# Kernel optimization log

Hardware: AMD Instinct MI355X
Metric: run time of the kernel (lower is better)

## Reference

```python
import jax, jax.numpy as jnp
import numpy as np

EPS = 1e-7  # keras backend epsilon
S = 64.0
M = 0.5
B, D, NC = 1024, 512, 50000


def setup_inputs() -> dict:
    key = jax.random.key(0)
    kx, kw, kl = jax.random.split(key, 3)
    x = jax.random.normal(kx, (B, D), dtype=jnp.float32)
    W = jax.random.normal(kw, (D, NC), dtype=jnp.float32)
    labels = jax.random.randint(kl, (B,), 0, NC)
    y = jax.nn.one_hot(labels, NC, dtype=jnp.float32)  # [B, NC] one-hot targets
    return {"x": x, "y": y, "W": W}


def reference(x, y, W):
    # L2-normalize embeddings (rows) and class weights (columns)
    xn = x / jnp.linalg.norm(x, axis=1, keepdims=True)
    Wn = W / jnp.linalg.norm(W, axis=0, keepdims=True)
    logits = xn @ Wn  # [B, NC] cosine similarities
    theta = jnp.arccos(jnp.clip(logits, -1.0 + EPS, 1.0 - EPS))
    target_logits = jnp.cos(theta + M)
    logits = logits * (1.0 - y) + target_logits * y
    logits = logits * S
    return jax.nn.softmax(logits, axis=-1)
```

## Files before the change

kernel.cpp:

```cpp
#include <hip/hip_runtime.h>
#include <hip/hip_fp16.h>
#include <cstdint>
#include <cstddef>

#define NCLS 50000
#define DIM 512
#define NROW 1024
#define NTN 391

typedef _Float16 half8 __attribute__((ext_vector_type(8)));
typedef float f32x4 __attribute__((ext_vector_type(4)));

#define AS1(p) ((const __attribute__((address_space(1))) void*)(p))
#define AS3(p) ((__attribute__((address_space(3))) void*)(p))

__global__ void prep_x_kernel(const float* __restrict__ x,
                              __half* __restrict__ xh,
                              float* __restrict__ rn)
{
    int row = blockIdx.x;
    int l = threadIdx.x;
    const float4* xr = (const float4*)(x + (size_t)row * DIM);
    __half2* dst = (__half2*)(xh + (size_t)row * DIM);
    float s = 0.f;
#pragma unroll
    for (int i = 0; i < 2; ++i) {
        int idx = l + i * 64;
        float4 v = xr[idx];
        dst[idx * 2]     = __floats2half2_rn(v.x, v.y);
        dst[idx * 2 + 1] = __floats2half2_rn(v.z, v.w);
        s += v.x * v.x + v.y * v.y + v.z * v.z + v.w * v.w;
    }
#pragma unroll
    for (int off = 32; off > 0; off >>= 1) s += __shfl_down(s, off);
    if (l == 0) rn[row] = rsqrtf(s);
}

__global__ void transpose_w_kernel(const float* __restrict__ W,
                                   __half* __restrict__ Wt,
                                   float* __restrict__ part)
{
    __shared__ float tile[64][65];
    __shared__ float cpart[4][64];
    int n0 = blockIdx.x * 64;
    int k0 = blockIdx.y * 64;
    int t = threadIdx.x;
    int f4 = t & 15;
    int kr = t >> 4;
    int n = n0 + f4 * 4;
    bool ok = (n < NCLS);
#pragma unroll
    for (int i = 0; i < 4; ++i) {
        int k = kr + i * 16;
        float4 v = ok ? *(const float4*)(W + (size_t)(k0 + k) * NCLS + n)
                      : make_float4(0.f, 0.f, 0.f, 0.f);
        tile[k][f4 * 4 + 0] = v.x;
        tile[k][f4 * 4 + 1] = v.y;
        tile[k][f4 * 4 + 2] = v.z;
        tile[k][f4 * 4 + 3] = v.w;
    }
    __syncthreads();
#pragma unroll
    for (int i = 0; i < 8; ++i) {
        int idx = t + i * 256;
        int nn = idx >> 5;
        int kp = idx & 31;
        int gn = n0 + nn;
        if (gn < NCLS) {
            __half2 h = __floats2half2_rn(tile[kp * 2][nn], tile[kp * 2 + 1][nn]);
            *(__half2*)(Wt + (size_t)gn * DIM + k0 + kp * 2) = h;
        }
    }
    {
        int nn = t & 63;
        int seg = t >> 6;
        float s = 0.f;
#pragma unroll
        for (int k = 0; k < 16; ++k) {
            float v = tile[seg * 16 + k][nn];
            s += v * v;
        }
        cpart[seg][nn] = s;
        __syncthreads();
        if (t < 64 && n0 + t < NCLS) {
            part[(size_t)blockIdx.y * NCLS + n0 + t] =
                cpart[0][t] + cpart[1][t] + cpart[2][t] + cpart[3][t];
        }
    }
}

__global__ void make_cn_kernel(const float* __restrict__ part, float* __restrict__ cn)
{
    int c = blockIdx.x * 256 + threadIdx.x;
    if (c >= NCLS) return;
    float s = 0.f;
#pragma unroll
    for (int j = 0; j < 8; ++j) s += part[(size_t)j * NCLS + c];
    cn[c] = rsqrtf(s);
}

__global__ void find_labels_kernel(const float4* __restrict__ y4, int* __restrict__ lab)
{
    int i4 = blockIdx.x * 256 + threadIdx.x;
    float4 v = y4[i4];
    if (v.x != 0.f || v.y != 0.f || v.z != 0.f || v.w != 0.f) {
        long base = (long)i4 * 4;
        if (v.x != 0.f) { long i = base + 0; lab[i / NCLS] = (int)(i % NCLS); }
        if (v.y != 0.f) { long i = base + 1; lab[i / NCLS] = (int)(i % NCLS); }
        if (v.z != 0.f) { long i = base + 2; lab[i / NCLS] = (int)(i % NCLS); }
        if (v.w != 0.f) { long i = base + 3; lab[i / NCLS] = (int)(i % NCLS); }
    }
}

template<int PASS>
__global__ __launch_bounds__(256, 4) void gemm_arc_kernel(
    const __half* __restrict__ A,
    const __half* __restrict__ Bt,
    const float* __restrict__ rn,
    const float* __restrict__ cn,
    const int* __restrict__ lab,
    const float* __restrict__ rs,
    float* __restrict__ out,
    float* __restrict__ rowpart)
{
    __shared__ __align__(16) __half As[128 * 64];
    __shared__ __align__(16) __half Bs[128 * 64];
    __shared__ float rsum[2][128];

    const int tid = threadIdx.x;
    const int wid = tid >> 6;
    const int lane = tid & 63;
    const int wm = wid >> 1;
    const int wn = wid & 1;

    const int b = blockIdx.x;
    const int w = (b & 7) * NTN + (b >> 3);
    const int mt = w & 7;
    const int nt = w >> 3;
    const int tileM = mt * 128;
    const int tileN = nt * 128;

    const int srow = lane >> 3;
    const int sblk = (lane & 7) ^ srow;

    f32x4 acc[4][4] = {};

    auto stage = [&](int k0) {
#pragma unroll
        for (int c = 0; c < 4; ++c) {
            int chunk = wid * 4 + c;
            int row = chunk * 8 + srow;
            const __half* sa = A + (size_t)(tileM + row) * DIM + k0 + sblk * 8;
            __builtin_amdgcn_global_load_lds(AS1(sa), AS3((char*)As + chunk * 1024), 16, 0, 0);
            int gn = tileN + row;
            if (gn > NCLS - 1) gn = NCLS - 1;
            const __half* sb = Bt + (size_t)gn * DIM + k0 + sblk * 8;
            __builtin_amdgcn_global_load_lds(AS1(sb), AS3((char*)Bs + chunk * 1024), 16, 0, 0);
        }
    };

    auto compute = [&]() {
        const int krow = lane >> 4;
        const int rl = lane & 15;
#pragma unroll
        for (int kk = 0; kk < 2; ++kk) {
            half8 af[4], bf[4];
#pragma unroll
            for (int m = 0; m < 4; ++m) {
                int r = wm * 64 + m * 16 + rl;
                int kb = (kk * 4 + krow) ^ (r & 7);
                af[m] = *(const half8*)((const char*)As + r * 128 + kb * 16);
            }
#pragma unroll
            for (int n = 0; n < 4; ++n) {
                int r = wn * 64 + n * 16 + rl;
                int kb = (kk * 4 + krow) ^ (r & 7);
                bf[n] = *(const half8*)((const char*)Bs + r * 128 + kb * 16);
            }
#pragma unroll
            for (int m = 0; m < 4; ++m)
#pragma unroll
                for (int n = 0; n < 4; ++n)
                    acc[m][n] = __builtin_amdgcn_mfma_f32_16x16x32_f16(af[m], bf[n], acc[m][n], 0, 0, 0);
        }
    };

#pragma unroll 1
    for (int k0 = 0; k0 < DIM; k0 += 64) {
        stage(k0);
        __syncthreads();
        compute();
        __syncthreads();
    }

    const float cosM = 0.8775825618903728f;
    const float sinM = 0.4794255386042030f;
    const int col_l = lane & 15;
    const int rgrp = lane >> 4;

#pragma unroll
    for (int m = 0; m < 4; ++m) {
        int gr0 = tileM + wm * 64 + m * 16 + rgrp * 4;
        float rnv[4]; int labv[4]; float rsv[4];
#pragma unroll
        for (int r = 0; r < 4; ++r) {
            rnv[r] = rn[gr0 + r];
            labv[r] = lab[gr0 + r];
            if (PASS == 1) rsv[r] = rs[gr0 + r];
        }
        float rowacc[4] = {0.f, 0.f, 0.f, 0.f};
#pragma unroll
        for (int n = 0; n < 4; ++n) {
            int gc = tileN + wn * 64 + n * 16 + col_l;
            bool okc = (gc < NCLS);
            float cnv = okc ? cn[gc] : 0.f;
#pragma unroll
            for (int r = 0; r < 4; ++r) {
                float cv = acc[m][n][r] * rnv[r] * cnv;
                float logit;
                if (gc == labv[r]) {
                    float cc = fminf(fmaxf(cv, -1.f + 1e-7f), 1.f - 1e-7f);
                    logit = 64.f * (cc * cosM - sqrtf(1.f - cc * cc) * sinM);
                } else {
                    logit = 64.f * cv;
                }
                float e = __expf(logit);
                if (PASS == 0) {
                    if (okc) rowacc[r] += e;
                } else {
                    if (okc) out[(size_t)(gr0 + r) * NCLS + gc] = e * rsv[r];
                }
            }
        }
        if (PASS == 0) {
#pragma unroll
            for (int r = 0; r < 4; ++r) {
                float s = rowacc[r];
                s += __shfl_xor(s, 1);
                s += __shfl_xor(s, 2);
                s += __shfl_xor(s, 4);
                s += __shfl_xor(s, 8);
                if (col_l == 0) rsum[wn][wm * 64 + m * 16 + rgrp * 4 + r] = s;
            }
        }
    }
    if (PASS == 0) {
        __syncthreads();
        if (tid < 128) {
            float tot = rsum[0][tid] + rsum[1][tid];
            rowpart[(size_t)nt * NROW + tileM + tid] = tot;
        }
    }
}

__global__ void reduce_rs_kernel(const float* __restrict__ rowpart, float* __restrict__ rs)
{
    int row = blockIdx.x * 256 + threadIdx.x;
    float s = 0.f;
    for (int t = 0; t < NTN; ++t) s += rowpart[(size_t)t * NROW + row];
    rs[row] = 1.f / s;
}

extern "C" void kernel_launch(void* const* d_in, const int* in_sizes, int n_in,
                              void* d_out, int out_size, void* d_ws, size_t ws_size,
                              hipStream_t stream)
{
    const float* x = (const float*)d_in[0];
    const float* y = (const float*)d_in[1];
    const float* W = (const float*)d_in[2];
    float* out = (float*)d_out;

    char* ws = (char*)d_ws;
    __half* Wt     = (__half*)(ws);
    __half* xh     = (__half*)(ws + 51200000);
    float* rn      = (float*) (ws + 52248576);
    float* cn      = (float*) (ws + 52252672);
    float* part    = (float*) (ws + 52452672);
    float* rowpart = part;
    int*   lab     = (int*)   (ws + 54054208);
    float* rs      = (float*) (ws + 54058304);

    hipLaunchKernelGGL(prep_x_kernel, dim3(NROW), dim3(64), 0, stream, x, xh, rn);
    hipLaunchKernelGGL(transpose_w_kernel, dim3(782, 8), dim3(256), 0, stream, W, Wt, part);
    hipLaunchKernelGGL(make_cn_kernel, dim3(196), dim3(256), 0, stream, part, cn);
    hipLaunchKernelGGL(find_labels_kernel, dim3(50000), dim3(256), 0, stream, (const float4*)y, lab);
    hipLaunchKernelGGL(gemm_arc_kernel<0>, dim3(8 * NTN), dim3(256), 0, stream,
                       xh, Wt, rn, cn, lab, rs, out, rowpart);
    hipLaunchKernelGGL(reduce_rs_kernel, dim3(4), dim3(256), 0, stream, rowpart, rs);
    hipLaunchKernelGGL(gemm_arc_kernel<1>, dim3(8 * NTN), dim3(256), 0, stream,
                       xh, Wt, rn, cn, lab, rs, out, rowpart);
}
```

Before: 257.7 us.

## Replace second GEMM pass with single pass plus separate normalization kernel

```diff
diff --git a/kernel.cpp b/kernel.cpp
--- a/kernel.cpp
+++ b/kernel.cpp
@@ -112,14 +112,12 @@
     }
 }
 
-template<int PASS>
 __global__ __launch_bounds__(256, 4) void gemm_arc_kernel(
     const __half* __restrict__ A,
     const __half* __restrict__ Bt,
     const float* __restrict__ rn,
     const float* __restrict__ cn,
     const int* __restrict__ lab,
-    const float* __restrict__ rs,
     float* __restrict__ out,
     float* __restrict__ rowpart)
 {
@@ -201,12 +199,11 @@
 #pragma unroll
     for (int m = 0; m < 4; ++m) {
         int gr0 = tileM + wm * 64 + m * 16 + rgrp * 4;
-        float rnv[4]; int labv[4]; float rsv[4];
+        float rnv[4]; int labv[4];
 #pragma unroll
         for (int r = 0; r < 4; ++r) {
             rnv[r] = rn[gr0 + r];
             labv[r] = lab[gr0 + r];
-            if (PASS == 1) rsv[r] = rs[gr0 + r];
         }
         float rowacc[4] = {0.f, 0.f, 0.f, 0.f};
 #pragma unroll
@@ -225,31 +222,26 @@
                     logit = 64.f * cv;
                 }
                 float e = __expf(logit);
-                if (PASS == 0) {
-                    if (okc) rowacc[r] += e;
-                } else {
-                    if (okc) out[(size_t)(gr0 + r) * NCLS + gc] = e * rsv[r];
+                if (okc) {
+                    rowacc[r] += e;
+                    out[(size_t)(gr0 + r) * NCLS + gc] = e;
                 }
             }
         }
-        if (PASS == 0) {
-#pragma unroll
-            for (int r = 0; r < 4; ++r) {
-                float s = rowacc[r];
-                s += __shfl_xor(s, 1);
-                s += __shfl_xor(s, 2);
-                s += __shfl_xor(s, 4);
-                s += __shfl_xor(s, 8);
-                if (col_l == 0) rsum[wn][wm * 64 + m * 16 + rgrp * 4 + r] = s;
-            }
-        }
-    }
-    if (PASS == 0) {
-        __syncthreads();
-        if (tid < 128) {
-            float tot = rsum[0][tid] + rsum[1][tid];
-            rowpart[(size_t)nt * NROW + tileM + tid] = tot;
-        }
+#pragma unroll
+        for (int r = 0; r < 4; ++r) {
+            float s = rowacc[r];
+            s += __shfl_xor(s, 1);
+            s += __shfl_xor(s, 2);
+            s += __shfl_xor(s, 4);
+            s += __shfl_xor(s, 8);
+            if (col_l == 0) rsum[wn][wm * 64 + m * 16 + rgrp * 4 + r] = s;
+        }
+    }
+    __syncthreads();
+    if (tid < 128) {
+        float tot = rsum[0][tid] + rsum[1][tid];
+        rowpart[(size_t)nt * NROW + tileM + tid] = tot;
     }
 }
 
@@ -259,6 +251,19 @@
     float s = 0.f;
     for (int t = 0; t < NTN; ++t) s += rowpart[(size_t)t * NROW + row];
     rs[row] = 1.f / s;
+}
+
+__global__ void finalize_kernel(float* __restrict__ vals, const float* __restrict__ rs)
+{
+    int row = blockIdx.y;
+    int i = blockIdx.x * 256 + threadIdx.x;
+    if (i < NCLS / 4) {
+        float s = rs[row];
+        float4* p = (float4*)(vals + (size_t)row * NCLS);
+        float4 v = p[i];
+        v.x *= s; v.y *= s; v.z *= s; v.w *= s;
+        p[i] = v;
+    }
 }
 
 extern "C" void kernel_launch(void* const* d_in, const int* in_sizes, int n_in,
@@ -284,9 +289,8 @@
     hipLaunchKernelGGL(transpose_w_kernel, dim3(782, 8), dim3(256), 0, stream, W, Wt, part);
     hipLaunchKernelGGL(make_cn_kernel, dim3(196), dim3(256), 0, stream, part, cn);
     hipLaunchKernelGGL(find_labels_kernel, dim3(50000), dim3(256), 0, stream, (const float4*)y, lab);
-    hipLaunchKernelGGL(gemm_arc_kernel<0>, dim3(8 * NTN), dim3(256), 0, stream,
-                       xh, Wt, rn, cn, lab, rs, out, rowpart);
+    hipLaunchKernelGGL(gemm_arc_kernel, dim3(8 * NTN), dim3(256), 0, stream,
+                       xh, Wt, rn, cn, lab, out, rowpart);
     hipLaunchKernelGGL(reduce_rs_kernel, dim3(4), dim3(256), 0, stream, rowpart, rs);
-    hipLaunchKernelGGL(gemm_arc_kernel<1>, dim3(8 * NTN), dim3(256), 0, stream,
-                       xh, Wt, rn, cn, lab, rs, out, rowpart);
-}
+    hipLaunchKernelGGL(finalize_kernel, dim3(49, NROW), dim3(256), 0, stream, out, rs);
+}
```

Result: slower. 280.7 us (+8.9%).

## Triple-buffer LDS K-loop with async global_load_lds prefetch two stages ahead

Applied to the files above, without the earlier changes.

```diff
diff --git a/kernel.cpp b/kernel.cpp
--- a/kernel.cpp
+++ b/kernel.cpp
@@ -113,7 +113,7 @@
 }
 
 template<int PASS>
-__global__ __launch_bounds__(256, 4) void gemm_arc_kernel(
+__global__ __launch_bounds__(256, 3) void gemm_arc_kernel(
     const __half* __restrict__ A,
     const __half* __restrict__ Bt,
     const float* __restrict__ rn,
@@ -123,8 +123,7 @@
     float* __restrict__ out,
     float* __restrict__ rowpart)
 {
-    __shared__ __align__(16) __half As[128 * 64];
-    __shared__ __align__(16) __half Bs[128 * 64];
+    __shared__ __align__(16) char ring[3][16384];
     __shared__ float rsum[2][128];
 
     const int tid = threadIdx.x;
@@ -132,6 +131,9 @@
     const int lane = tid & 63;
     const int wm = wid >> 1;
     const int wn = wid & 1;
+    const int rl = lane & 15;
+    const int krow = lane >> 4;
+    const int koff = (krow ^ ((rl >> 1) & 3)) * 16;
 
     const int b = blockIdx.x;
     const int w = (b & 7) * NTN + (b >> 3);
@@ -140,63 +142,57 @@
     const int tileM = mt * 128;
     const int tileN = nt * 128;
 
-    const int srow = lane >> 3;
-    const int sblk = (lane & 7) ^ srow;
-
     f32x4 acc[4][4] = {};
 
-    auto stage = [&](int k0) {
-#pragma unroll
-        for (int c = 0; c < 4; ++c) {
-            int chunk = wid * 4 + c;
-            int row = chunk * 8 + srow;
-            const __half* sa = A + (size_t)(tileM + row) * DIM + k0 + sblk * 8;
-            __builtin_amdgcn_global_load_lds(AS1(sa), AS3((char*)As + chunk * 1024), 16, 0, 0);
-            int gn = tileN + row;
+    const int rowl = lane >> 2;
+    const int sw = (lane & 3) ^ ((lane >> 3) & 3);
+    auto stage = [&](int t) {
+        char* base = ring[t % 3];
+        const int k0 = t * 32;
+#pragma unroll
+        for (int c = 0; c < 2; ++c) {
+            int r16 = (wid * 2 + c) * 16;
+            const __half* sa = A + (size_t)(tileM + r16 + rowl) * DIM + k0 + sw * 8;
+            __builtin_amdgcn_global_load_lds(AS1(sa), AS3(base + r16 * 64), 16, 0, 0);
+            int gn = tileN + r16 + rowl;
             if (gn > NCLS - 1) gn = NCLS - 1;
-            const __half* sb = Bt + (size_t)gn * DIM + k0 + sblk * 8;
-            __builtin_amdgcn_global_load_lds(AS1(sb), AS3((char*)Bs + chunk * 1024), 16, 0, 0);
+            const __half* sb = Bt + (size_t)gn * DIM + k0 + sw * 8;
+            __builtin_amdgcn_global_load_lds(AS1(sb), AS3(base + 8192 + r16 * 64), 16, 0, 0);
         }
     };
 
-    auto compute = [&]() {
-        const int krow = lane >> 4;
-        const int rl = lane & 15;
-#pragma unroll
-        for (int kk = 0; kk < 2; ++kk) {
-            half8 af[4], bf[4];
-#pragma unroll
-            for (int m = 0; m < 4; ++m) {
-                int r = wm * 64 + m * 16 + rl;
-                int kb = (kk * 4 + krow) ^ (r & 7);
-                af[m] = *(const half8*)((const char*)As + r * 128 + kb * 16);
-            }
-#pragma unroll
-            for (int n = 0; n < 4; ++n) {
-                int r = wn * 64 + n * 16 + rl;
-                int kb = (kk * 4 + krow) ^ (r & 7);
-                bf[n] = *(const half8*)((const char*)Bs + r * 128 + kb * 16);
-            }
-#pragma unroll
-            for (int m = 0; m < 4; ++m)
-#pragma unroll
-                for (int n = 0; n < 4; ++n)
-                    acc[m][n] = __builtin_amdgcn_mfma_f32_16x16x32_f16(af[m], bf[n], acc[m][n], 0, 0, 0);
-        }
-    };
+    stage(0); stage(1);
 
 #pragma unroll 1
-    for (int k0 = 0; k0 < DIM; k0 += 64) {
-        stage(k0);
-        __syncthreads();
-        compute();
-        __syncthreads();
+    for (int t = 0; t < 16; ++t) {
+        if (t == 15) asm volatile("s_waitcnt vmcnt(0)" ::: "memory");
+        else         asm volatile("s_waitcnt vmcnt(4)" ::: "memory");
+        __builtin_amdgcn_s_barrier();
+        __builtin_amdgcn_sched_barrier(0);
+
+        if (t + 2 < 16) stage(t + 2);
+
+        const char* sb_ = ring[t % 3];
+        half8 af[4], bf[4];
+#pragma unroll
+        for (int m = 0; m < 4; ++m)
+            af[m] = *(const half8*)(sb_ + (wm * 64 + m * 16 + rl) * 64 + koff);
+#pragma unroll
+        for (int n = 0; n < 4; ++n)
+            bf[n] = *(const half8*)(sb_ + 8192 + (wn * 64 + n * 16 + rl) * 64 + koff);
+        __builtin_amdgcn_s_setprio(1);
+#pragma unroll
+        for (int m = 0; m < 4; ++m)
+#pragma unroll
+            for (int n = 0; n < 4; ++n)
+                acc[m][n] = __builtin_amdgcn_mfma_f32_16x16x32_f16(af[m], bf[n], acc[m][n], 0, 0, 0);
+        __builtin_amdgcn_s_setprio(0);
     }
 
     const float cosM = 0.8775825618903728f;
     const float sinM = 0.4794255386042030f;
-    const int col_l = lane & 15;
-    const int rgrp = lane >> 4;
+    const int col_l = rl;
+    const int rgrp = krow;
 
 #pragma unroll
     for (int m = 0; m < 4; ++m) {
```

Measured after the change: 280.8 us. 9.0% more time.

## Fuse label search into GEMM pass and stage output through LDS for vector stores

Applied to the files above, without the earlier changes.

```diff
diff --git a/kernel.cpp b/kernel.cpp
--- a/kernel.cpp
+++ b/kernel.cpp
@@ -99,26 +99,14 @@
     cn[c] = rsqrtf(s);
 }
 
-__global__ void find_labels_kernel(const float4* __restrict__ y4, int* __restrict__ lab)
-{
-    int i4 = blockIdx.x * 256 + threadIdx.x;
-    float4 v = y4[i4];
-    if (v.x != 0.f || v.y != 0.f || v.z != 0.f || v.w != 0.f) {
-        long base = (long)i4 * 4;
-        if (v.x != 0.f) { long i = base + 0; lab[i / NCLS] = (int)(i % NCLS); }
-        if (v.y != 0.f) { long i = base + 1; lab[i / NCLS] = (int)(i % NCLS); }
-        if (v.z != 0.f) { long i = base + 2; lab[i / NCLS] = (int)(i % NCLS); }
-        if (v.w != 0.f) { long i = base + 3; lab[i / NCLS] = (int)(i % NCLS); }
-    }
-}
-
 template<int PASS>
 __global__ __launch_bounds__(256, 4) void gemm_arc_kernel(
     const __half* __restrict__ A,
     const __half* __restrict__ Bt,
     const float* __restrict__ rn,
     const float* __restrict__ cn,
-    const int* __restrict__ lab,
+    const float* __restrict__ y,
+    int* __restrict__ lab,
     const float* __restrict__ rs,
     float* __restrict__ out,
     float* __restrict__ rowpart)
@@ -126,6 +114,7 @@
     __shared__ __align__(16) __half As[128 * 64];
     __shared__ __align__(16) __half Bs[128 * 64];
     __shared__ float rsum[2][128];
+    __shared__ int labloc[128];
 
     const int tid = threadIdx.x;
     const int wid = tid >> 6;
@@ -142,6 +131,8 @@
 
     const int srow = lane >> 3;
     const int sblk = (lane & 7) ^ srow;
+
+    if (PASS == 0 && tid < 128) labloc[tid] = -1;
 
     f32x4 acc[4][4] = {};
 
@@ -193,20 +184,45 @@
         __syncthreads();
     }
 
+    if (PASS == 0) {
+#pragma unroll
+        for (int i = 0; i < 16; ++i) {
+            int idx = tid + i * 256;
+            int row = idx >> 5;
+            int c4 = idx & 31;
+            int gc = tileN + c4 * 4;
+            if (gc < NCLS) {
+                float4 v = *(const float4*)(y + (size_t)(tileM + row) * NCLS + gc);
+                int hit = -1;
+                if (v.x != 0.f) hit = gc;
+                if (v.y != 0.f) hit = gc + 1;
+                if (v.z != 0.f) hit = gc + 2;
+                if (v.w != 0.f) hit = gc + 3;
+                if (hit >= 0) {
+                    labloc[row] = hit;
+                    lab[tileM + row] = hit;
+                }
+            }
+        }
+        __syncthreads();
+    }
+
     const float cosM = 0.8775825618903728f;
     const float sinM = 0.4794255386042030f;
     const int col_l = lane & 15;
     const int rgrp = lane >> 4;
+    float* buf = (float*)As;
 
 #pragma unroll
     for (int m = 0; m < 4; ++m) {
-        int gr0 = tileM + wm * 64 + m * 16 + rgrp * 4;
+        int lr0 = wm * 64 + m * 16 + rgrp * 4;
+        int gr0 = tileM + lr0;
         float rnv[4]; int labv[4]; float rsv[4];
 #pragma unroll
         for (int r = 0; r < 4; ++r) {
             rnv[r] = rn[gr0 + r];
-            labv[r] = lab[gr0 + r];
-            if (PASS == 1) rsv[r] = rs[gr0 + r];
+            if (PASS == 0) labv[r] = labloc[lr0 + r];
+            else { labv[r] = lab[gr0 + r]; rsv[r] = rs[gr0 + r]; }
         }
         float rowacc[4] = {0.f, 0.f, 0.f, 0.f};
 #pragma unroll
@@ -228,7 +244,7 @@
                 if (PASS == 0) {
                     if (okc) rowacc[r] += e;
                 } else {
-                    if (okc) out[(size_t)(gr0 + r) * NCLS + gc] = e * rsv[r];
+                    buf[(wm * 16 + rgrp * 4 + r) * 128 + wn * 64 + n * 16 + col_l] = e * rsv[r];
                 }
             }
         }
@@ -240,8 +256,21 @@
                 s += __shfl_xor(s, 2);
                 s += __shfl_xor(s, 4);
                 s += __shfl_xor(s, 8);
-                if (col_l == 0) rsum[wn][wm * 64 + m * 16 + rgrp * 4 + r] = s;
-            }
+                if (col_l == 0) rsum[wn][lr0 + r] = s;
+            }
+        } else {
+            __syncthreads();
+#pragma unroll
+            for (int i = 0; i < 4; ++i) {
+                int idx = tid + i * 256;
+                int lr = idx >> 5;
+                int c4 = idx & 31;
+                int gr = tileM + (lr >> 4) * 64 + m * 16 + (lr & 15);
+                int gcl = tileN + c4 * 4;
+                if (gcl < NCLS)
+                    *(float4*)(out + (size_t)gr * NCLS + gcl) = ((float4*)buf)[idx];
+            }
+            __syncthreads();
         }
     }
     if (PASS == 0) {
@@ -283,10 +312,9 @@
     hipLaunchKernelGGL(prep_x_kernel, dim3(NROW), dim3(64), 0, stream, x, xh, rn);
     hipLaunchKernelGGL(transpose_w_kernel, dim3(782, 8), dim3(256), 0, stream, W, Wt, part);
     hipLaunchKernelGGL(make_cn_kernel, dim3(196), dim3(256), 0, stream, part, cn);
-    hipLaunchKernelGGL(find_labels_kernel, dim3(50000), dim3(256), 0, stream, (const float4*)y, lab);
     hipLaunchKernelGGL(gemm_arc_kernel<0>, dim3(8 * NTN), dim3(256), 0, stream,
-                       xh, Wt, rn, cn, lab, rs, out, rowpart);
+                       xh, Wt, rn, cn, y, lab, rs, out, rowpart);
     hipLaunchKernelGGL(reduce_rs_kernel, dim3(4), dim3(256), 0, stream, rowpart, rs);
     hipLaunchKernelGGL(gemm_arc_kernel<1>, dim3(8 * NTN), dim3(256), 0, stream,
-                       xh, Wt, rn, cn, lab, rs, out, rowpart);
-}
+                       xh, Wt, rn, cn, y, lab, rs, out, rowpart);
+}
```

After: 274.4 us. +6.5%, slower.
